# Performance work log

Hardware: AMD Instinct MI355X
Metric: run time of the kernel (lower is better)

The kernel has to match this reference:

```python
import jax, jax.numpy as jnp
import numpy as np

B, H, S, D = 4, 16, 2048, 64

def setup_inputs() -> dict:
    key = jax.random.key(0)
    k1, k2, k3 = jax.random.split(key, 3)
    Q = jax.random.normal(k1, (B, H, S, D), dtype=jnp.float32)
    K = jax.random.normal(k2, (B, H, S, D), dtype=jnp.float32)
    V = jax.random.normal(k3, (B, H, S, D), dtype=jnp.float32)
    # causal boolean mask, broadcast over batch/heads
    mask = jnp.tril(jnp.ones((S, S), dtype=bool))
    return {"Q": Q, "K": K, "V": V, "mask": mask}

def reference(Q, K, V, mask):
    d_k = Q.shape[-1]
    # [..., m, n] score matrix
    qk = jnp.einsum('...md,...nd->...mn', Q, K) / jnp.sqrt(jnp.float32(d_k))
    neg_inf = jnp.float32(-jnp.inf)
    scores = qk + jnp.where(mask, jnp.float32(0.0), neg_inf)
    # numerically stable softmax over last dim (matches SoftmaxModule)
    probs = jax.nn.softmax(scores, axis=-1)
    return jnp.einsum('...mn,...nd->...md', probs, V)
```

## Files before the change

kernel.cpp:

```cpp
#include <hip/hip_runtime.h>

#define S_LEN 2048
#define D_DIM 64
#define BM    128
#define BN    64
#define NW    4
#define NT    (NW * 64)
#define BH    64
#define QB    (S_LEN / BM)

typedef __attribute__((ext_vector_type(2)))  __fp16   fp16x2;
typedef __attribute__((ext_vector_type(4)))  _Float16 half4;
typedef __attribute__((ext_vector_type(8)))  _Float16 half8;
typedef __attribute__((ext_vector_type(16))) float    f32x16;

#define MFMA3216(a, b, c) __builtin_amdgcn_mfma_f32_32x32x16_f16((a), (b), (c), 0, 0, 0)


union H8 { half4 q[2]; half8 o; };
union PK2 { fp16x2 f; _Float16 h[2]; };

__device__ __forceinline__ half4 pk4(float a, float b, float c, float d) {
  PK2 lo, hi;
  lo.f = __builtin_amdgcn_cvt_pkrtz(a, b);
  hi.f = __builtin_amdgcn_cvt_pkrtz(c, d);
  half4 r; r[0] = lo.h[0]; r[1] = lo.h[1]; r[2] = hi.h[0]; r[3] = hi.h[1];
  return r;
}

__device__ __forceinline__ void subtile(const _Float16 (*kh)[68],
                                        const _Float16 (*vT)[68],
                                        const half8* qf,
                                        f32x16& o0, f32x16& o1, float& l,
                                        int s, int qc, int h,
                                        bool domask, int diff) {
  f32x16 st;
#pragma unroll
  for (int e = 0; e < 16; ++e) st[e] = 0.f;
#pragma unroll
  for (int c = 0; c < 4; ++c) {
    H8 kf;
    kf.q[0] = *(const half4*)&kh[32 * s + qc][16 * c + 8 * h];
    kf.q[1] = *(const half4*)&kh[32 * s + qc][16 * c + 8 * h + 4];
    st = MFMA3216(kf.o, qf[c], st);
  }
  if (domask) {
#pragma unroll
    for (int e = 0; e < 16; ++e) {
      int keyl = (e & 3) + 8 * (e >> 2) + 4 * h;
      if (keyl > diff) st[e] = -1e30f;
    }
  }
#pragma unroll
  for (int e = 0; e < 16; ++e) st[e] = exp2f(st[e]);
  float ts = 0.f;
#pragma unroll
  for (int e = 0; e < 16; ++e) ts += st[e];
  l += ts;
#pragma unroll
  for (int cl = 0; cl < 2; ++cl) {
    half8 pf;
#pragma unroll
    for (int j = 0; j < 8; j += 2) {
      PK2 pp;
      pp.f = __builtin_amdgcn_cvt_pkrtz(st[8 * cl + j], st[8 * cl + j + 1]);
      pf[j] = pp.h[0]; pf[j + 1] = pp.h[1];
    }
    const int c = 2 * s + cl;
    H8 v0, v1;
    v0.q[0] = *(const half4*)&vT[qc][16 * c + 8 * h];
    v0.q[1] = *(const half4*)&vT[qc][16 * c + 8 * h + 4];
    v1.q[0] = *(const half4*)&vT[32 + qc][16 * c + 8 * h];
    v1.q[1] = *(const half4*)&vT[32 + qc][16 * c + 8 * h + 4];
    o0 = MFMA3216(v0.o, pf, o0);
    o1 = MFMA3216(v1.o, pf, o1);
  }
}

__global__ __launch_bounds__(NT) void fa_fwd(const float* __restrict__ Q,
                                             const float* __restrict__ K,
                                             const float* __restrict__ V,
                                             float* __restrict__ Out) {
  __shared__ _Float16 kh[BN][68];
  __shared__ _Float16 vT[D_DIM][68];

  const int tid  = threadIdx.x;
  const int wave = tid >> 6;
  const int lane = tid & 63;
  const int h    = lane >> 5;
  const int qc   = lane & 31;

  const int bid = blockIdx.x;
  const int bh  = bid & (BH - 1);
  const int qb  = (QB - 1) - (bid >> 6);
  const int q0  = qb * BM;
  const int q0w = q0 + wave * 32;
  const long base = (long)bh * S_LEN * D_DIM;

  const float SCALE = 0.125f * 1.44269504088896340736f;

  half8 qf[4];
  {
    const float* qp = Q + base + (long)(q0w + qc) * D_DIM;
#pragma unroll
    for (int c = 0; c < 4; ++c) {
      float4 u = *(const float4*)(qp + 16 * c + 8 * h);
      float4 v = *(const float4*)(qp + 16 * c + 8 * h + 4);
      half4 a = pk4(u.x * SCALE, u.y * SCALE, u.z * SCALE, u.w * SCALE);
      half4 b = pk4(v.x * SCALE, v.y * SCALE, v.z * SCALE, v.w * SCALE);
      H8 t; t.q[0] = a; t.q[1] = b;
      qf[c] = t.o;
    }
  }

  f32x16 o0, o1;
#pragma unroll
  for (int e = 0; e < 16; ++e) { o0[e] = 0.f; o1[e] = 0.f; }
  float l = 0.f;

  const int T     = (q0 + BM) / BN;
  const int myEnd = q0w + 31;

  const int skey = tid >> 2, sc = (tid & 3) * 16;
  const int sd   = tid & 63, sr = tid >> 6;
  const float* kp = K + base + (long)skey * D_DIM + sc;
  const float* vp = V + base + (long)(16 * sr) * D_DIM + sd;

  float4 kreg[4];
  float  vreg[16];
  const int inv[4] = {0, 2, 1, 3};

  {
#pragma unroll
    for (int j = 0; j < 4; ++j) kreg[j] = *(const float4*)(kp + 4 * j);
#pragma unroll
    for (int j = 0; j < 16; ++j) vreg[j] = vp[(long)j * D_DIM];
    kp += BN * D_DIM; vp += BN * D_DIM;
#pragma unroll
    for (int j = 0; j < 4; ++j)
      *(half4*)&kh[skey][sc + 4 * j] = pk4(kreg[j].x, kreg[j].y, kreg[j].z, kreg[j].w);
#pragma unroll
    for (int p = 0; p < 4; ++p) {
      int kb = inv[p] * 4;
      *(half4*)&vT[sd][16 * sr + 4 * p] = pk4(vreg[kb], vreg[kb + 1], vreg[kb + 2], vreg[kb + 3]);
    }
  }
  __syncthreads();

  for (int t = 0; t < T; ++t) {
    const int n0 = t * BN;

    if (t + 1 < T) {
#pragma unroll
      for (int j = 0; j < 4; ++j) kreg[j] = *(const float4*)(kp + 4 * j);
#pragma unroll
      for (int j = 0; j < 16; ++j) vreg[j] = vp[(long)j * D_DIM];
      kp += BN * D_DIM; vp += BN * D_DIM;
    }

    if (n0 + BN <= q0w) {
      subtile(kh, vT, qf, o0, o1, l, 0, qc, h, false, 0);
      subtile(kh, vT, qf, o0, o1, l, 1, qc, h, false, 0);
    } else if (n0 <= myEnd) {
#pragma unroll
      for (int s = 0; s < 2; ++s) {
        const int sbase = n0 + 32 * s;
        if (sbase > myEnd) break;
        if (sbase + 31 > q0w)
          subtile(kh, vT, qf, o0, o1, l, s, qc, h, true, q0w + qc - sbase);
        else
          subtile(kh, vT, qf, o0, o1, l, s, qc, h, false, 0);
      }
    }

    __syncthreads();
    if (t + 1 < T) {
#pragma unroll
      for (int j = 0; j < 4; ++j)
        *(half4*)&kh[skey][sc + 4 * j] = pk4(kreg[j].x, kreg[j].y, kreg[j].z, kreg[j].w);
#pragma unroll
      for (int p = 0; p < 4; ++p) {
        int kb = inv[p] * 4;
        *(half4*)&vT[sd][16 * sr + 4 * p] = pk4(vreg[kb], vreg[kb + 1], vreg[kb + 2], vreg[kb + 3]);
      }
    }
    __syncthreads();
  }

  l += __shfl_xor(l, 32);
  const float invl = 1.0f / l;
  float* op = Out + base + (long)(q0w + qc) * D_DIM;
#pragma unroll
  for (int e = 0; e < 16; ++e) {
    int d = (e & 3) + 8 * (e >> 2) + 4 * h;
    op[d]      = o0[e] * invl;
    op[32 + d] = o1[e] * invl;
  }
}

extern "C" void kernel_launch(void* const* d_in, const int* in_sizes, int n_in,
                              void* d_out, int out_size, void* d_ws, size_t ws_size,
                              hipStream_t stream) {
  const float* Q = (const float*)d_in[0];
  const float* K = (const float*)d_in[1];
  const float* V = (const float*)d_in[2];
  (void)in_sizes; (void)n_in; (void)d_ws; (void)ws_size; (void)out_size;
  float* Out = (float*)d_out;
  dim3 grid(BH * QB);
  dim3 block(NT);
  hipLaunchKernelGGL(fa_fwd, grid, block, 0, stream, Q, K, V, Out);
}
```

Measured before the change: 203.8 us.

## Halve query tile to 64 rows with two waves, drop register prefetch pipeline

Reduces the query block from 128 to 64 rows and the workgroup from four waves to two. That doubles the grid and lets each diagonal tile be handled with a fixed mask pattern. The register-staged prefetch of the next K/V tile is removed: each iteration now loads, converts and stores the tile to LDS between two barriers. The V transpose is rewritten to pack pairs of keys into fp16x2 stores. Other changes are exp2 via raw v_exp_f32 inline asm and precomputed LDS byte pointers. The trade-off is less global-load/compute overlap inside a block in exchange for more blocks and finer causal granularity.

```diff
diff --git a/kernel.cpp b/kernel.cpp
--- a/kernel.cpp
+++ b/kernel.cpp
@@ -2,9 +2,9 @@
 
 #define S_LEN 2048
 #define D_DIM 64
-#define BM    128
+#define BM    64
 #define BN    64
-#define NW    4
+#define NW    2
 #define NT    (NW * 64)
 #define BH    64
 #define QB    (S_LEN / BM)
@@ -17,8 +17,14 @@
 #define MFMA3216(a, b, c) __builtin_amdgcn_mfma_f32_32x32x16_f16((a), (b), (c), 0, 0, 0)
 
 
-union H8 { half4 q[2]; half8 o; };
+union H8  { half4 q[2]; half8 o; };
 union PK2 { fp16x2 f; _Float16 h[2]; };
+
+__device__ __forceinline__ float fexp2(float x) {
+  float r;
+  asm("v_exp_f32 %0, %1" : "=v"(r) : "v"(x));
+  return r;
+}
 
 __device__ __forceinline__ half4 pk4(float a, float b, float c, float d) {
   PK2 lo, hi;
@@ -28,20 +34,18 @@
   return r;
 }
 
-__device__ __forceinline__ void subtile(const _Float16 (*kh)[68],
-                                        const _Float16 (*vT)[68],
+__device__ __forceinline__ void subtile(const char* kb, const char* vb,
                                         const half8* qf,
                                         f32x16& o0, f32x16& o1, float& l,
-                                        int s, int qc, int h,
-                                        bool domask, int diff) {
+                                        int s, int h, bool domask, int diff) {
   f32x16 st;
 #pragma unroll
   for (int e = 0; e < 16; ++e) st[e] = 0.f;
 #pragma unroll
   for (int c = 0; c < 4; ++c) {
     H8 kf;
-    kf.q[0] = *(const half4*)&kh[32 * s + qc][16 * c + 8 * h];
-    kf.q[1] = *(const half4*)&kh[32 * s + qc][16 * c + 8 * h + 4];
+    kf.q[0] = *(const half4*)(kb + 4352 * s + 32 * c);
+    kf.q[1] = *(const half4*)(kb + 4352 * s + 32 * c + 8);
     st = MFMA3216(kf.o, qf[c], st);
   }
   if (domask) {
@@ -52,11 +56,10 @@
     }
   }
 #pragma unroll
-  for (int e = 0; e < 16; ++e) st[e] = exp2f(st[e]);
-  float ts = 0.f;
-#pragma unroll
-  for (int e = 0; e < 16; ++e) ts += st[e];
-  l += ts;
+  for (int e = 0; e < 16; ++e) st[e] = fexp2(st[e]);
+  float a = ((st[0] + st[1]) + (st[2] + st[3])) + ((st[4] + st[5]) + (st[6] + st[7]));
+  float b = ((st[8] + st[9]) + (st[10] + st[11])) + ((st[12] + st[13]) + (st[14] + st[15]));
+  l += a + b;
 #pragma unroll
   for (int cl = 0; cl < 2; ++cl) {
     half8 pf;
@@ -68,10 +71,10 @@
     }
     const int c = 2 * s + cl;
     H8 v0, v1;
-    v0.q[0] = *(const half4*)&vT[qc][16 * c + 8 * h];
-    v0.q[1] = *(const half4*)&vT[qc][16 * c + 8 * h + 4];
-    v1.q[0] = *(const half4*)&vT[32 + qc][16 * c + 8 * h];
-    v1.q[1] = *(const half4*)&vT[32 + qc][16 * c + 8 * h + 4];
+    v0.q[0] = *(const half4*)(vb + 32 * c);
+    v0.q[1] = *(const half4*)(vb + 32 * c + 8);
+    v1.q[0] = *(const half4*)(vb + 4352 + 32 * c);
+    v1.q[1] = *(const half4*)(vb + 4352 + 32 * c + 8);
     o0 = MFMA3216(v0.o, pf, o0);
     o1 = MFMA3216(v1.o, pf, o1);
   }
@@ -118,73 +121,60 @@
   for (int e = 0; e < 16; ++e) { o0[e] = 0.f; o1[e] = 0.f; }
   float l = 0.f;
 
-  const int T     = (q0 + BM) / BN;
-  const int myEnd = q0w + 31;
-
-  const int skey = tid >> 2, sc = (tid & 3) * 16;
-  const int sd   = tid & 63, sr = tid >> 6;
+  const int T = qb + 1;
+
+  const int skey = tid >> 1, sc = (tid & 1) * 32;
   const float* kp = K + base + (long)skey * D_DIM + sc;
-  const float* vp = V + base + (long)(16 * sr) * D_DIM + sd;
-
-  float4 kreg[4];
-  float  vreg[16];
-  const int inv[4] = {0, 2, 1, 3};
-
-  {
-#pragma unroll
-    for (int j = 0; j < 4; ++j) kreg[j] = *(const float4*)(kp + 4 * j);
-#pragma unroll
-    for (int j = 0; j < 16; ++j) vreg[j] = vp[(long)j * D_DIM];
-    kp += BN * D_DIM; vp += BN * D_DIM;
-#pragma unroll
-    for (int j = 0; j < 4; ++j)
-      *(half4*)&kh[skey][sc + 4 * j] = pk4(kreg[j].x, kreg[j].y, kreg[j].z, kreg[j].w);
-#pragma unroll
-    for (int p = 0; p < 4; ++p) {
-      int kb = inv[p] * 4;
-      *(half4*)&vT[sd][16 * sr + 4 * p] = pk4(vreg[kb], vreg[kb + 1], vreg[kb + 2], vreg[kb + 3]);
-    }
-  }
-  __syncthreads();
+  const int vk0 = (tid >> 2) * 2, vdg = tid & 3;
+  const int vq  = (vk0 >> 2) & 3;
+  const int vqs = ((vq & 1) << 1) | (vq >> 1);
+  const int vpos = (vk0 & 48) | (vqs << 2) | (vk0 & 3);
+  const float* vp = V + base + (long)vk0 * D_DIM + vdg * 16;
+
+  const char* kb = (const char*)&kh[qc][8 * h];
+  const char* vb = (const char*)&vT[qc][8 * h];
 
   for (int t = 0; t < T; ++t) {
-    const int n0 = t * BN;
+    __syncthreads();
+    {
+#pragma unroll
+      for (int j = 0; j < 8; ++j) {
+        float4 a = *(const float4*)(kp + 4 * j);
+        *(half4*)&kh[skey][sc + 4 * j] = pk4(a.x, a.y, a.z, a.w);
+      }
+    }
+    {
+      float4 va[4], vbq[4];
+#pragma unroll
+      for (int j = 0; j < 4; ++j) {
+        va[j]  = *(const float4*)(vp + 4 * j);
+        vbq[j] = *(const float4*)(vp + D_DIM + 4 * j);
+      }
+#pragma unroll
+      for (int j = 0; j < 4; ++j) {
+        const float* aj = (const float*)&va[j];
+        const float* bj = (const float*)&vbq[j];
+#pragma unroll
+        for (int i = 0; i < 4; ++i) {
+          PK2 w;
+          w.f = __builtin_amdgcn_cvt_pkrtz(aj[i], bj[i]);
+          *(fp16x2*)&vT[vdg * 16 + 4 * j + i][vpos] = w.f;
+        }
+      }
+    }
+    kp += BN * D_DIM;
+    vp += BN * D_DIM;
+    __syncthreads();
 
     if (t + 1 < T) {
-#pragma unroll
-      for (int j = 0; j < 4; ++j) kreg[j] = *(const float4*)(kp + 4 * j);
-#pragma unroll
-      for (int j = 0; j < 16; ++j) vreg[j] = vp[(long)j * D_DIM];
-      kp += BN * D_DIM; vp += BN * D_DIM;
-    }
-
-    if (n0 + BN <= q0w) {
-      subtile(kh, vT, qf, o0, o1, l, 0, qc, h, false, 0);
-      subtile(kh, vT, qf, o0, o1, l, 1, qc, h, false, 0);
-    } else if (n0 <= myEnd) {
-#pragma unroll
-      for (int s = 0; s < 2; ++s) {
-        const int sbase = n0 + 32 * s;
-        if (sbase > myEnd) break;
-        if (sbase + 31 > q0w)
-          subtile(kh, vT, qf, o0, o1, l, s, qc, h, true, q0w + qc - sbase);
-        else
-          subtile(kh, vT, qf, o0, o1, l, s, qc, h, false, 0);
-      }
-    }
-
-    __syncthreads();
-    if (t + 1 < T) {
-#pragma unroll
-      for (int j = 0; j < 4; ++j)
-        *(half4*)&kh[skey][sc + 4 * j] = pk4(kreg[j].x, kreg[j].y, kreg[j].z, kreg[j].w);
-#pragma unroll
-      for (int p = 0; p < 4; ++p) {
-        int kb = inv[p] * 4;
-        *(half4*)&vT[sd][16 * sr + 4 * p] = pk4(vreg[kb], vreg[kb + 1], vreg[kb + 2], vreg[kb + 3]);
-      }
-    }
-    __syncthreads();
+      subtile(kb, vb, qf, o0, o1, l, 0, h, false, 0);
+      subtile(kb, vb, qf, o0, o1, l, 1, h, false, 0);
+    } else if (wave == 0) {
+      subtile(kb, vb, qf, o0, o1, l, 0, h, true, qc);
+    } else {
+      subtile(kb, vb, qf, o0, o1, l, 0, h, false, 0);
+      subtile(kb, vb, qf, o0, o1, l, 1, h, true, qc);
+    }
   }
 
   l += __shfl_xor(l, 32);
```

Result: slower. 237.0 us (+16.3%).
